# Optimization experiments

Measured on AMD Instinct MI355X. Metric: run time of the kernel, lower is better.

Reference implementation:

```python
import math
import jax, jax.numpy as jnp
import numpy as np

V, D, DEPTH, S, B = 32000, 1024, 4, 512, 2
N, K = 16, 4            # ssm state_dim, d_conv
R = math.ceil(D / 16)   # dt_rank ('auto') = 64
MLP = 4 * D


def _ln(x, s, b):
    m = jnp.mean(x, -1, keepdims=True)
    v = jnp.mean((x - m) ** 2, -1, keepdims=True)
    return (x - m) * jax.lax.rsqrt(v + 1e-5) * s + b


def _dwconv(x, w):
    # x: [B,S,D], w: [D,1,K]; causal depthwise conv (torch pads K-1 both sides then slices [:S])
    xt = jnp.transpose(x, (0, 2, 1))  # [B,D,S]
    y = jax.lax.conv_general_dilated(
        xt, w, window_strides=(1,), padding=[(K - 1, 0)],
        feature_group_count=D, dimension_numbers=('NCH', 'OIH', 'NCH'))
    return jnp.transpose(y, (0, 2, 1))


def _ssm(x, zw, pw, cw, dw, db, al, dpar, ow):
    z = x @ zw.T                     # [B,S,D]
    p = x @ pw.T                     # [B,S,R+2N]
    dt_un, Bp, Cp = p[..., :R], p[..., R:R + N], p[..., R + N:]
    dt = jax.nn.softplus(dt_un @ dw.T + db)          # [B,S,D]
    u = jax.nn.silu(_dwconv(x, cw))                  # [B,S,D]
    A = -jnp.exp(al)                                 # [D,N]
    At = jnp.exp(dt[..., None] * A)                  # [B,S,D,N]
    Bt = jnp.where(jnp.abs(A) < 1e-8, dt[..., None], (At - 1.0) / (A + 1e-10))
    inp = jnp.einsum('bsdn,bsn,bsd->bsdn', Bt, Bp, u)

    def step(h, xs):
        At_t, inp_t, C_t = xs
        h = At_t * h + inp_t
        return h, jnp.einsum('bn,bdn->bd', C_t, h)

    h0 = jnp.zeros((x.shape[0], D, N), x.dtype)
    _, ys = jax.lax.scan(step, h0, (jnp.moveaxis(At, 1, 0), jnp.moveaxis(inp, 1, 0), jnp.moveaxis(Cp, 1, 0)))
    y = jnp.moveaxis(ys, 0, 1)                       # [B,S,D]
    y = (y + u * dpar) * jax.nn.silu(z)
    return y @ ow.T


def _forward(input_ids, timesteps, tok_emb, time_w1, time_b1, time_w2, time_b2,
             norm1_s, norm1_b, xW, zW, pW, convW, dtW, dtb, A_log, Dp, outW,
             norm2_s, norm2_b, mlpW1, mlpb1, mlpW2, mlpb2, normo_s, normo_b, headW, headb):
    half = D // 2
    inv = jnp.exp(-(math.log(10000.0) / half) * jnp.arange(half, dtype=jnp.float32))
    args = timesteps.astype(jnp.float32)[:, None] * inv
    temb = jnp.concatenate([jnp.sin(args), jnp.cos(args)], axis=-1)        # [B,D]
    temb = jax.nn.silu(temb @ time_w1.T + time_b1) @ time_w2.T + time_b2
    x = tok_emb[input_ids] + temb[:, None, :]                              # [B,S,D]

    def block(x, prm):
        n1s, n1b, zw, pw, cw, dw, db, al, dpar, ow, n2s, n2b, w1, b1, w2, b2 = prm
        x = x + _ssm(_ln(x, n1s, n1b), zw, pw, cw, dw, db, al, dpar, ow)
        xn = _ln(x, n2s, n2b)
        x = x + (jax.nn.gelu(xn @ w1.T + b1, approximate=False) @ w2.T + b2)
        return x, None

    stacked = (norm1_s, norm1_b, zW, pW, convW, dtW, dtb, A_log, Dp, outW,
               norm2_s, norm2_b, mlpW1, mlpb1, mlpW2, mlpb2)
    x, _ = jax.lax.scan(block, x, stacked)
    x = _ln(x, normo_s, normo_b)
    return x @ headW.T + headb  # [B,S,V]


def setup_inputs():
    key = jax.random.key(0)
    ks = jax.random.split(key, 24)
    rn = lambda k, sh, sc=0.02: jax.random.normal(k, sh, jnp.float32) * sc
    dt_std = R ** (-0.5) * 0.1
    inp = {
        'input_ids': jax.random.randint(ks[0], (B, S), 0, V + 1),
        'timesteps': jax.random.randint(ks[1], (B,), 0, 100),
        'tok_emb': rn(ks[2], (V + 1, D)),
        'time_w1': rn(ks[3], (4 * D, D)), 'time_b1': jnp.zeros((4 * D,), jnp.float32),
        'time_w2': rn(ks[4], (D, 4 * D)), 'time_b2': jnp.zeros((D,), jnp.float32),
        'norm1_s': jnp.ones((DEPTH, D), jnp.float32), 'norm1_b': jnp.zeros((DEPTH, D), jnp.float32),
        'xW': rn(ks[5], (DEPTH, D, D)),   # in_proj_x (dead in forward, grad=0)
        'zW': rn(ks[6], (DEPTH, D, D)),
        'pW': rn(ks[7], (DEPTH, R + 2 * N, D)),
        'convW': rn(ks[8], (DEPTH, D, 1, K), 0.1),
        'dtW': jax.random.uniform(ks[9], (DEPTH, D, R), jnp.float32, -dt_std, dt_std),
        'dtb': jnp.full((DEPTH, D), math.log(math.expm1(0.001)), jnp.float32),
        'A_log': jnp.tile(jnp.log(jnp.arange(1, N + 1, dtype=jnp.float32))[None, None, :], (DEPTH, D, 1)),
        'Dp': jnp.ones((DEPTH, D), jnp.float32),
        'outW': rn(ks[10], (DEPTH, D, D)),
        'norm2_s': jnp.ones((DEPTH, D), jnp.float32), 'norm2_b': jnp.zeros((DEPTH, D), jnp.float32),
        'mlpW1': rn(ks[11], (DEPTH, MLP, D)), 'mlpb1': jnp.zeros((DEPTH, MLP), jnp.float32),
        'mlpW2': rn(ks[12], (DEPTH, D, MLP)), 'mlpb2': jnp.zeros((DEPTH, D), jnp.float32),
        'normo_s': jnp.ones((D,), jnp.float32), 'normo_b': jnp.zeros((D,), jnp.float32),
        'headW': rn(ks[13], (V, D)), 'headb': jnp.zeros((V,), jnp.float32),
    }
    return inp


def reference(input_ids, timesteps, tok_emb, time_w1, time_b1, time_w2, time_b2,
              norm1_s, norm1_b, xW, zW, pW, convW, dtW, dtb, A_log, Dp, outW,
              norm2_s, norm2_b, mlpW1, mlpb1, mlpW2, mlpb2, normo_s, normo_b, headW, headb):
    return _forward(input_ids, timesteps, tok_emb, time_w1, time_b1, time_w2, time_b2,
                    norm1_s, norm1_b, xW, zW, pW, convW, dtW, dtb, A_log, Dp, outW,
                    norm2_s, norm2_b, mlpW1, mlpb1, mlpW2, mlpb2, normo_s, normo_b, headW, headb)
```

## Files before the change

### kernel.cpp

```cpp
#include <hip/hip_runtime.h>
#include <math.h>


#define DEV __device__ __forceinline__
typedef unsigned int u32;
typedef unsigned short ushort;
typedef __bf16 bf16x8 __attribute__((ext_vector_type(8)));
typedef float f32x4 __attribute__((ext_vector_type(4)));
typedef ushort us8 __attribute__((ext_vector_type(8)));

DEV float silu_f(float x){ return x / (1.f + expf(-x)); }
DEV float gelu_f(float x){ return 0.5f * x * (1.f + erff(x * 0.70710678118654752f)); }
DEV float softplus_f(float x){ return (x > 20.f) ? x : log1pf(expf(x)); }
DEV ushort f2b(float f){
  u32 u = __builtin_bit_cast(u32, f);
  return (ushort)((u + 0x7fffu + ((u >> 16) & 1u)) >> 16);
}
DEV float b2f(ushort u){ return __builtin_bit_cast(float, (u32)u << 16); }

DEV void gl_lds16(const ushort* g, ushort* l){
  __builtin_amdgcn_global_load_lds(
      (const __attribute__((address_space(1))) u32*)g,
      (__attribute__((address_space(3))) u32*)l, 16, 0, 0);
}

DEV us8 cvt2(float4 a, float4 b){
  us8 v;
  v[0]=f2b(a.x); v[1]=f2b(a.y); v[2]=f2b(a.z); v[3]=f2b(a.w);
  v[4]=f2b(b.x); v[5]=f2b(b.y); v[6]=f2b(b.z); v[7]=f2b(b.w);
  return v;
}

DEV void cvt_layer_unit(u32 j, const float* zWl, const float* pWl, const float* oWl,
                        const float* m1Wl, const float* m2Wl, ushort* wl)
{
  const float* src; u32 sj, dj;
  if (j < 294912u){
    dj = j;
    u32 row = j >> 8;
    if (row < 1024u){ src = zWl; sj = j; }
    else {
      u32 pr = row - 1024u;
      if (pr >= 96u){ ushort4 z4 = {0,0,0,0}; ((ushort4*)wl)[dj] = z4; return; }
      src = pWl; sj = pr*256u + (j & 255u);
    }
  } else if (j < 557056u){ u32 k = j - 294912u;  dj = j; src = oWl;  sj = k; }
  else if (j < 1605632u){ u32 k = j - 557056u;  dj = j; src = m1Wl; sj = k; }
  else                  { u32 k = j - 1605632u; dj = j; src = m2Wl; sj = k; }
  float4 v = ((const float4*)src)[sj];
  ushort4 o4; o4.x=f2b(v.x); o4.y=f2b(v.y); o4.z=f2b(v.z); o4.w=f2b(v.w);
  ((ushort4*)wl)[dj] = o4;
}

__global__ __launch_bounds__(256) void k_cvtmega(
    const float* __restrict__ zW, const float* __restrict__ pW,
    const float* __restrict__ oW, const float* __restrict__ m1W,
    const float* __restrict__ m2W, ushort* __restrict__ wall)
{
  u32 i = blockIdx.x*256u + threadIdx.x;
  if (i >= 10616832u) return;
  u32 l = i / 2654208u;
  u32 j = i - l*2654208u;
  cvt_layer_unit(j, zW + (size_t)l*1048576u, pW + (size_t)l*98304u,
                 oW + (size_t)l*1048576u, m1W + (size_t)l*4194304u,
                 m2W + (size_t)l*4194304u, wall + (size_t)l*10616832u);
}

__global__ __launch_bounds__(256) void k_cvtall(
    const float* __restrict__ zWl, const float* __restrict__ pWl,
    const float* __restrict__ oWl, const float* __restrict__ m1Wl,
    const float* __restrict__ m2Wl, ushort* __restrict__ wl)
{
  u32 j = blockIdx.x*256u + threadIdx.x;
  if (j >= 2654208u) return;
  cvt_layer_unit(j, zWl, pWl, oWl, m1Wl, m2Wl, wl);
}

__global__ __launch_bounds__(256) void k_cvt(const float* __restrict__ in, ushort* __restrict__ out, int n4){
  int i = blockIdx.x*256 + threadIdx.x;
  if (i >= n4) return;
  float4 v = ((const float4*)in)[i];
  ushort4 o; o.x=f2b(v.x); o.y=f2b(v.y); o.z=f2b(v.z); o.w=f2b(v.w);
  ((ushort4*)out)[i] = o;
}

__global__ __launch_bounds__(256) void k_temb1m(const int* __restrict__ ts, const float* __restrict__ w1,
                                                const float* __restrict__ b1, float* __restrict__ t1){
  __shared__ float sXT[1024];
  int bid = blockIdx.x;
  int tid = threadIdx.x;
  int b = (bid*4) >> 12;
  float tv = (float)ts[b];
  #pragma unroll
  for (int k=0;k<4;k++){
    int j = tid + k*256;
    int i = j & 511;
    float arg = tv * expf(-(9.210340371976184f/512.f) * (float)i);
    sXT[j] = (j < 512) ? sinf(arg) : cosf(arg);
  }
  __syncthreads();
  int o = bid*4 + (tid >> 6);
  int lane = tid & 63;
  int j = o & 4095;
  const float4* xr = (const float4*)sXT;
  const float4* wr = (const float4*)(w1 + (size_t)j*1024);
  float acc = 0.f;
  #pragma unroll
  for (int i=0;i<4;i++){
    float4 x4 = xr[i*64 + lane], w4 = wr[i*64 + lane];
    acc += x4.x*w4.x + x4.y*w4.y + x4.z*w4.z + x4.w*w4.w;
  }
  #pragma unroll
  for (int off=32; off; off>>=1) acc += __shfl_down(acc, off);
  if (lane==0) t1[o] = silu_f(acc + b1[j]);
}

__global__ __launch_bounds__(256) void k_temb2(const float* __restrict__ t1, const float* __restrict__ w2,
                                               const float* __restrict__ b2, float* __restrict__ t2){
  int o = blockIdx.x*4 + (threadIdx.x >> 6);
  int lane = threadIdx.x & 63;
  int b = o >> 10, j = o & 1023;
  const float4* xr = (const float4*)(t1 + b*4096);
  const float4* wr = (const float4*)(w2 + (size_t)j*4096);
  float acc = 0.f;
  #pragma unroll
  for (int i=0;i<16;i++){
    float4 x4 = xr[i*64 + lane], w4 = wr[i*64 + lane];
    acc += x4.x*w4.x + x4.y*w4.y + x4.z*w4.z + x4.w*w4.w;
  }
  #pragma unroll
  for (int off=32; off; off>>=1) acc += __shfl_down(acc, off);
  if (lane==0) t2[o] = acc + b2[j];
}

DEV void ln_body(float4 v, const float* sc, const float* bi, int row, int t,
                 float* o, ushort* obf)
{
  float sum = v.x+v.y+v.z+v.w;
  float sq  = v.x*v.x+v.y*v.y+v.z*v.z+v.w*v.w;
  for (int o_=32;o_;o_>>=1){ sum += __shfl_down(sum,o_); sq += __shfl_down(sq,o_); }
  __shared__ float ps[8];
  int lane = t & 63, wid = t >> 6;
  if (lane==0){ ps[wid]=sum; ps[4+wid]=sq; }
  __syncthreads();
  float tot = ps[0]+ps[1]+ps[2]+ps[3];
  float tsq = ps[4]+ps[5]+ps[6]+ps[7];
  float m = tot * (1.f/1024.f);
  float var = tsq*(1.f/1024.f) - m*m;
  float r = rsqrtf(var + 1e-5f);
  float4 s4 = ((const float4*)sc)[t];
  float4 b4 = ((const float4*)bi)[t];
  float4 o4;
  o4.x = (v.x-m)*r*s4.x + b4.x;
  o4.y = (v.y-m)*r*s4.y + b4.y;
  o4.z = (v.z-m)*r*s4.z + b4.z;
  o4.w = (v.w-m)*r*s4.w + b4.w;
  ((float4*)(o + (size_t)row*1024))[t] = o4;
  ushort4 ob; ob.x=f2b(o4.x); ob.y=f2b(o4.y); ob.z=f2b(o4.z); ob.w=f2b(o4.w);
  ((ushort4*)(obf + (size_t)row*1024))[t] = ob;
}

__global__ __launch_bounds__(256) void k_ln(const float* __restrict__ x, const float* __restrict__ sc,
                                            const float* __restrict__ bi, float* __restrict__ o,
                                            ushort* __restrict__ obf){
  int row = blockIdx.x, t = threadIdx.x;
  float4 v = ((const float4*)(x + (size_t)row*1024))[t];
  ln_body(v, sc, bi, row, t, o, obf);
}

__global__ __launch_bounds__(256) void k_embln(const int* __restrict__ ids, const float* __restrict__ tok,
                                               const float* __restrict__ t2, const float* __restrict__ sc,
                                               const float* __restrict__ bi, float* __restrict__ xout,
                                               float* __restrict__ o, ushort* __restrict__ obf){
  int row = blockIdx.x, t = threadIdx.x;
  int id = ids[row];
  float4 v = ((const float4*)(tok + (size_t)id*1024))[t];
  float4 e = ((const float4*)(t2 + ((row >> 9) << 10)))[t];
  v.x += e.x; v.y += e.y; v.z += e.z; v.w += e.w;
  ((float4*)(xout + (size_t)row*1024))[t] = v;
  ln_body(v, sc, bi, row, t, o, obf);
}

__global__ __launch_bounds__(512) void k_scanf(
    const ushort* __restrict__ pb64, const float* __restrict__ dtW, const float* __restrict__ dtb,
    const float* __restrict__ xn, const float* __restrict__ p, const float* __restrict__ alog,
    const float* __restrict__ z, const float* __restrict__ Dp,
    const float* __restrict__ cw, ushort* __restrict__ y2b)
{
  const int bid = blockIdx.x;
  const int logical = (bid & 7)*256 + (bid >> 3);
  const int d = logical & 1023;
  const int b = logical >> 10;
  const int tid = threadIdx.x;
  const int c = tid >> 4, n = tid & 15;
  const float al = alog[d*16 + n];
  const float A = -expf(al);
  const float invA = 1.f/(A + 1e-10f);
  const bool tiny = fabsf(A) < 1e-8f;
  const float dscale = Dp[d];
  const float cw0 = cw[d*4], cw1 = cw[d*4+1], cw2 = cw[d*4+2], cw3 = cw[d*4+3];
  const size_t base = (size_t)b*512*1024 + d;
  const float* pp = p + (size_t)b*512*96;
  const int s0 = c*16;

  __shared__ float sXN[520];
  __shared__ float sDT[512], sZ[512];
  __shared__ float sA[512], sB[512], sH[512];
  __shared__ float sDTW[64];

  if (tid < 64) sDTW[tid] = dtW[d*64 + tid];
  {
    int s = tid - 3;
    sXN[tid] = (s >= 0) ? xn[base + (size_t)s*1024] : 0.f;
    if (tid < 3) sXN[512 + tid] = xn[base + (size_t)(509 + tid)*1024];
    sZ[tid] = z[base + (size_t)tid*1024];
  }
  __syncthreads();

  {
    const us8* pr = (const us8*)(pb64 + (size_t)(b*512 + tid)*64);
    float acc = 0.f;
    #pragma unroll
    for (int q=0;q<8;q++){
      us8 v = pr[q];
      #pragma unroll
      for (int e=0;e<8;e++)
        acc = fmaf(b2f(v[e]), sDTW[q*8+e], acc);
    }
    sDT[tid] = softplus_f(acc + dtb[d]);
  }
  __syncthreads();

  float At[16], inp[16];
  float h = 0.f, pa = 1.f;
  #pragma unroll
  for (int s8=0; s8<16; s8++){
    int s = s0 + s8;
    float uv = silu_f(sXN[s]*cw0 + sXN[s+1]*cw1 + sXN[s+2]*cw2 + sXN[s+3]*cw3);
    float dtv = sDT[s];
    float Bpv = pp[s*96 + 64 + n];
    float a  = expf(dtv*A);
    float bt = tiny ? dtv : (a-1.f)*invA;
    At[s8] = a;
    float ip = bt*Bpv*uv;
    inp[s8] = ip;
    h = a*h + ip;
    pa *= a;
  }
  sA[tid]=pa; sB[tid]=h;
  __syncthreads();
  if (tid < 16){
    float H = 0.f;
    #pragma unroll
    for (int c2=0;c2<32;c2++){
      sH[c2*16+tid] = H;
      H = sA[c2*16+tid]*H + sB[c2*16+tid];
    }
  }
  __syncthreads();

  h = sH[tid];
  #pragma unroll
  for (int s8=0; s8<16; s8++){
    int s = s0 + s8;
    h = At[s8]*h + inp[s8];
    float Cpv = pp[s*96 + 80 + n];
    float cc = Cpv*h;
    cc += __shfl_xor(cc,1);
    cc += __shfl_xor(cc,2);
    cc += __shfl_xor(cc,4);
    cc += __shfl_xor(cc,8);
    if (n==0){
      float uv = silu_f(sXN[s]*cw0 + sXN[s+1]*cw1 + sXN[s+2]*cw2 + sXN[s+3]*cw3);
      float zv = sZ[s];
      y2b[base + (size_t)s*1024] = f2b((cc + uv*dscale) * (zv/(1.f+expf(-zv))));
    }
  }
}

template<int TM, int TN, int EPI, bool OBF>
__global__ __launch_bounds__(256) void k_bgemm(
    const ushort* __restrict__ A,
    const ushort* __restrict__ W,
    const float* __restrict__ bias,
    const float* __restrict__ resid,
    void* __restrict__ Cout,
    int ldc, int nmax, int K,
    float* __restrict__ pout, ushort* __restrict__ pbout)
{
  constexpr int WN = 2;
  constexpr int WM = 2;
  constexpr int MR = TM/(WM*16);
  constexpr int NR = TN/(WN*16);

  __shared__ ushort As[TM*64] __attribute__((aligned(16)));
  __shared__ ushort Bs[TN*64] __attribute__((aligned(16)));
  const int t = threadIdx.x;
  const int w = t >> 6, lane = t & 63;
  const int wn = w % WN, wm = w / WN;
  const int m0 = blockIdx.y * TM;
  const int n0 = blockIdx.x * TN;

  f32x4 acc[MR][NR];
  #pragma unroll
  for (int i=0;i<MR;i++)
    #pragma unroll
    for (int j=0;j<NR;j++) acc[i][j] = (f32x4){0.f,0.f,0.f,0.f};

  const int srow = (lane >> 3);
  const int scol = (((lane & 7) ^ srow)) * 8;

  for (int k0 = 0; k0 < K; k0 += 64){
    __syncthreads();
    #pragma unroll
    for (int i=0;i<TM/32;i++){
      int chunk = i*4 + w;
      int row = chunk*8 + srow;
      gl_lds16(A + (size_t)(m0 + row)*K + k0 + scol, &As[chunk*512]);
    }
    #pragma unroll
    for (int i=0;i<TN/32;i++){
      int chunk = i*4 + w;
      int row = chunk*8 + srow;
      gl_lds16(W + (size_t)(n0 + row)*K + k0 + scol, &Bs[chunk*512]);
    }
    __syncthreads();
    const int fr = lane & 15;
    const int hi = lane >> 4;
    #pragma unroll
    for (int kk=0; kk<2; ++kk){
      bf16x8 a[MR], b[NR];
      const int cofs = (((kk<<2) | hi) ^ (fr & 7)) * 8;
      #pragma unroll
      for (int am=0; am<MR; am++)
        a[am] = *(const bf16x8*)&As[(wm*(MR*16) + am*16 + fr)*64 + cofs];
      #pragma unroll
      for (int bn=0; bn<NR; bn++)
        b[bn] = *(const bf16x8*)&Bs[(wn*(NR*16) + bn*16 + fr)*64 + cofs];
      #pragma unroll
      for (int am=0; am<MR; am++)
        #pragma unroll
        for (int bn=0; bn<NR; bn++)
          acc[am][bn] = __builtin_amdgcn_mfma_f32_16x16x32_bf16(a[am], b[bn], acc[am][bn], 0, 0, 0);
    }
  }

  #pragma unroll
  for (int am=0; am<MR; am++){
    #pragma unroll
    for (int bn=0; bn<NR; bn++){
      int r0 = m0 + wm*(MR*16) + am*16 + ((lane>>4)<<2);
      int cc = n0 + wn*(NR*16) + bn*16 + (lane&15);
      if (cc >= nmax) continue;
      float bv = 0.f;
      if constexpr (EPI==1 || EPI==2 || EPI==5) bv = bias[cc];
      #pragma unroll
      for (int r=0; r<4; r++){
        float v = acc[am][bn][r];
        if constexpr (EPI==1 || EPI==2 || EPI==5) v += bv;
        if constexpr (EPI==2) v = gelu_f(v);
        if constexpr (EPI==4 || EPI==5) v += resid[(size_t)(r0+r)*ldc + cc];
        if constexpr (EPI==6){
          if (cc < 1024) ((float*)Cout)[(size_t)(r0+r)*ldc + cc] = v;
          else {
            int pc = cc - 1024;
            if (pc < 96) pout[(size_t)(r0+r)*96 + pc] = v;
            if (pc < 64) pbout[(size_t)(r0+r)*64 + pc] = f2b(v);
          }
        } else if constexpr (OBF){
          ((ushort*)Cout)[(size_t)(r0+r)*ldc + cc] = f2b(v);
        } else {
          ((float*)Cout)[(size_t)(r0+r)*ldc + cc] = v;
        }
      }
    }
  }
}

__global__ __launch_bounds__(512) void k_bgemmHF(
    const ushort* __restrict__ A,
    const float*  __restrict__ W,
    const float* __restrict__ bias,
    float* __restrict__ Cout,
    int ldc, int K)
{
  __shared__ ushort As[256*64] __attribute__((aligned(16)));
  __shared__ ushort Bs[128*64] __attribute__((aligned(16)));
  const int t = threadIdx.x;
  const int w = t >> 6, lane = t & 63;
  const int wn = w & 1, wm = w >> 1;
  const int bid = blockIdx.x;
  const int logical = (bid & 7)*125 + (bid >> 3);
  const int m0 = (logical & 3) * 256;
  const int n0 = (logical >> 2) * 128;

  f32x4 acc[4][4];
  #pragma unroll
  for (int i=0;i<4;i++)
    #pragma unroll
    for (int j=0;j<4;j++) acc[i][j] = (f32x4){0.f,0.f,0.f,0.f};

  const int srow = (lane >> 3);
  const int scolA = (((lane & 7) ^ srow)) * 8;

  const int brow = t >> 2;
  const int bq   = t & 3;
  const float* wp = W + (size_t)(n0 + brow)*K + bq*16;
  const int slot0 = ((bq*2)   ^ (brow & 7)) * 8;
  const int slot1 = ((bq*2+1) ^ (brow & 7)) * 8;

  float4 fb[4];
  #pragma unroll
  for (int j=0;j<4;j++) fb[j] = *(const float4*)(wp + j*4);

  for (int k0 = 0; k0 < K; k0 += 64){
    __syncthreads();
    #pragma unroll
    for (int i=0;i<4;i++){
      int chunk = i*8 + w;
      int row = chunk*8 + srow;
      gl_lds16(A + (size_t)(m0 + row)*K + k0 + scolA, &As[chunk*512]);
    }
    *(us8*)&Bs[brow*64 + slot0] = cvt2(fb[0], fb[1]);
    *(us8*)&Bs[brow*64 + slot1] = cvt2(fb[2], fb[3]);
    if (k0 + 64 < K){
      #pragma unroll
      for (int j=0;j<4;j++) fb[j] = *(const float4*)(wp + k0 + 64 + j*4);
      asm volatile("s_waitcnt vmcnt(4) lgkmcnt(0)" ::: "memory");
    } else {
      asm volatile("s_waitcnt vmcnt(0) lgkmcnt(0)" ::: "memory");
    }
    __builtin_amdgcn_sched_barrier(0);
    __builtin_amdgcn_s_barrier();
    __builtin_amdgcn_sched_barrier(0);
    const int fr = lane & 15;
    const int hi = lane >> 4;
    #pragma unroll
    for (int kk=0; kk<2; ++kk){
      bf16x8 a[4], b[4];
      const int cofs = (((kk<<2) | hi) ^ (fr & 7)) * 8;
      #pragma unroll
      for (int am=0; am<4; am++)
        a[am] = *(const bf16x8*)&As[(wm*64 + am*16 + fr)*64 + cofs];
      #pragma unroll
      for (int bn=0; bn<4; bn++)
        b[bn] = *(const bf16x8*)&Bs[(wn*64 + bn*16 + fr)*64 + cofs];
      #pragma unroll
      for (int am=0; am<4; am++)
        #pragma unroll
        for (int bn=0; bn<4; bn++)
          acc[am][bn] = __builtin_amdgcn_mfma_f32_16x16x32_bf16(a[am], b[bn], acc[am][bn], 0, 0, 0);
    }
  }

  #pragma unroll
  for (int am=0; am<4; am++){
    #pragma unroll
    for (int bn=0; bn<4; bn++){
      int r0 = m0 + wm*64 + am*16 + ((lane>>4)<<2);
      int cc = n0 + wn*64 + bn*16 + (lane&15);
      float bv = bias[cc];
      #pragma unroll
      for (int r=0; r<4; r++)
        Cout[(size_t)(r0+r)*ldc + cc] = acc[am][bn][r] + bv;
    }
  }
}

extern "C" void kernel_launch(void* const* d_in, const int* in_sizes, int n_in,
                              void* d_out, int out_size, void* d_ws, size_t ws_size,
                              hipStream_t stream)
{
  const int*   ids    = (const int*)d_in[0];
  const int*   tsteps = (const int*)d_in[1];
  const float* tok    = (const float*)d_in[2];
  const float* tw1    = (const float*)d_in[3];
  const float* tb1    = (const float*)d_in[4];
  const float* tw2    = (const float*)d_in[5];
  const float* tb2    = (const float*)d_in[6];
  const float* n1s    = (const float*)d_in[7];
  const float* n1b    = (const float*)d_in[8];
  const float* zW     = (const float*)d_in[10];
  const float* pW     = (const float*)d_in[11];
  const float* cW     = (const float*)d_in[12];
  const float* dtW    = (const float*)d_in[13];
  const float* dtb    = (const float*)d_in[14];
  const float* alog   = (const float*)d_in[15];
  const float* Dp     = (const float*)d_in[16];
  const float* oW     = (const float*)d_in[17];
  const float* n2s    = (const float*)d_in[18];
  const float* n2b    = (const float*)d_in[19];
  const float* m1W    = (const float*)d_in[20];
  const float* m1b    = (const float*)d_in[21];
  const float* m2W    = (const float*)d_in[22];
  const float* m2b    = (const float*)d_in[23];
  const float* nos    = (const float*)d_in[24];
  const float* nob    = (const float*)d_in[25];
  const float* hW     = (const float*)d_in[26];
  const float* hb     = (const float*)d_in[27];

  float* ws = (float*)d_ws;
  float*  x    = ws;
  float*  xn   = ws + 1048576;
  float*  z    = ws + 2097152;
  float*  p    = ws + 3145728;
  ushort* pb64 = (ushort*)(ws + 3244032);
  float*  t1   = ws + 3276800;
  float*  t2   = ws + 3284992;
  ushort* xnb  = (ushort*)(ws + 3670016);
  ushort* y2b  = (ushort*)(ws + 4194304);
  ushort* h1b  = (ushort*)(ws + 5242880);

  const size_t WBASE = 7340032;
  const size_t WL_US = 10616832;
  const bool big = ws_size >= 179830784ull;
  ushort* wall = (ushort*)(ws + WBASE);
  ushort* whb  = (ushort*)(ws + WBASE + (big ? 4*(WL_US/2) : 0));

  dim3 blk(256);
  if (big)
    k_cvtmega<<<dim3(41472), blk, 0, stream>>>(zW, pW, oW, m1W, m2W, wall);
  k_temb1m<<<dim3(2048), blk, 0, stream>>>(tsteps, tw1, tb1, t1);
  k_temb2<<<dim3(512),  blk, 0, stream>>>(t1, tw2, tb2, t2);

  for (int l=0; l<4; l++){
    ushort* wl = wall + (big ? (size_t)l*WL_US : 0);
    ushort* wzp = wl;
    ushort* wo  = wl + 1179648;
    ushort* wm1 = wl + 2228224;
    ushort* wm2 = wl + 6422528;
    if (!big)
      k_cvtall<<<dim3(10368), blk, 0, stream>>>(
          zW + (size_t)l*1048576, pW + (size_t)l*98304, oW + (size_t)l*1048576,
          m1W + (size_t)l*4194304, m2W + (size_t)l*4194304, wl);
    if (l == 0)
      k_embln<<<dim3(1024), blk, 0, stream>>>(ids, tok, t2, n1s, n1b, x, xn, xnb);
    else
      k_ln<<<dim3(1024), blk, 0, stream>>>(x, n1s + l*1024, n1b + l*1024, xn, xnb);
    k_bgemm<64,64,6,false><<<dim3(18,16), blk, 0, stream>>>(xnb, wzp, nullptr, nullptr, z,
                                                            1024, 1152, 1024, p, pb64);
    k_scanf<<<dim3(2048), dim3(512), 0, stream>>>(pb64, dtW + (size_t)l*65536, dtb + l*1024,
                                                  xn, p, alog + l*16384, z, Dp + l*1024,
                                                  cW + l*4096, y2b);
    k_bgemm<64,64,4,false><<<dim3(16,16), blk, 0, stream>>>(y2b, wo, nullptr, x, x,
                                                            1024, 1024, 1024, nullptr, nullptr);
    k_ln<<<dim3(1024), blk, 0, stream>>>(x, n2s + l*1024, n2b + l*1024, xn, xnb);
    k_bgemm<64,64,2,true><<<dim3(64,16), blk, 0, stream>>>(xnb, wm1, m1b + l*4096, nullptr, h1b,
                                                           4096, 4096, 1024, nullptr, nullptr);
    k_bgemm<64,64,5,false><<<dim3(16,16), blk, 0, stream>>>(h1b, wm2, m2b + l*1024, x, x,
                                                            1024, 1024, 4096, nullptr, nullptr);
  }
  k_ln<<<dim3(1024), blk, 0, stream>>>(x, nos, nob, xn, xnb);

  if (big){
    k_bgemmHF<<<dim3(1000), dim3(512), 0, stream>>>(xnb, hW, hb, (float*)d_out, 32000, 1024);
  } else {
    for (int h=0; h<2; h++){
      k_cvt<<<dim3(16000), blk, 0, stream>>>(hW + (size_t)h*16384000, whb, 4096000);
      k_bgemm<128,128,1,false><<<dim3(125,8), blk, 0, stream>>>(xnb, whb, hb + h*16000, nullptr,
                                                                (float*)d_out + h*16000,
                                                                32000, 16000, 1024, nullptr, nullptr);
    }
  }
}
```

Measured before the change: 890.9 us.

## Double-buffer LDS tiles in bf16 GEMM to overlap global loads with MFMA

The GEMM kernel now keeps two LDS buffers per operand and issues the async global-to-LDS loads for the next K-step before computing on the current one. Explicit vmcnt waits and barriers replace the two __syncthreads per iteration. This is meant to hide global memory latency behind MFMA work, at the cost of twice the shared memory per block, which may reduce occupancy.

```diff
diff --git a/kernel.cpp b/kernel.cpp
--- a/kernel.cpp
+++ b/kernel.cpp
@@ -292,9 +292,12 @@
   constexpr int WM = 2;
   constexpr int MR = TM/(WM*16);
   constexpr int NR = TN/(WN*16);
-
-  __shared__ ushort As[TM*64] __attribute__((aligned(16)));
-  __shared__ ushort Bs[TN*64] __attribute__((aligned(16)));
+  constexpr int LA = TM/32;
+  constexpr int LB = TN/32;
+  constexpr int LT = LA + LB;
+
+  __shared__ ushort As[2][TM*64] __attribute__((aligned(16)));
+  __shared__ ushort Bs[2][TN*64] __attribute__((aligned(16)));
   const int t = threadIdx.x;
   const int w = t >> 6, lane = t & 63;
   const int wn = w % WN, wm = w / WN;
@@ -310,39 +313,54 @@
   const int srow = (lane >> 3);
   const int scol = (((lane & 7) ^ srow)) * 8;
 
-  for (int k0 = 0; k0 < K; k0 += 64){
-    __syncthreads();
-    #pragma unroll
-    for (int i=0;i<TM/32;i++){
+  auto issue = [&](int k0, int buf){
+    #pragma unroll
+    for (int i=0;i<LA;i++){
       int chunk = i*4 + w;
       int row = chunk*8 + srow;
-      gl_lds16(A + (size_t)(m0 + row)*K + k0 + scol, &As[chunk*512]);
-    }
-    #pragma unroll
-    for (int i=0;i<TN/32;i++){
+      gl_lds16(A + (size_t)(m0 + row)*K + k0 + scol, &As[buf][chunk*512]);
+    }
+    #pragma unroll
+    for (int i=0;i<LB;i++){
       int chunk = i*4 + w;
       int row = chunk*8 + srow;
-      gl_lds16(W + (size_t)(n0 + row)*K + k0 + scol, &Bs[chunk*512]);
-    }
-    __syncthreads();
-    const int fr = lane & 15;
-    const int hi = lane >> 4;
+      gl_lds16(W + (size_t)(n0 + row)*K + k0 + scol, &Bs[buf][chunk*512]);
+    }
+  };
+
+  issue(0, 0);
+  const int NS = K >> 6;
+  const int fr = lane & 15;
+  const int hi = lane >> 4;
+  for (int s = 0; s < NS; ++s){
+    const int cur = s & 1;
+    if (s + 1 < NS){
+      issue((s+1)*64, cur^1);
+      asm volatile("s_waitcnt vmcnt(%0)" :: "i"(LT) : "memory");
+    } else {
+      asm volatile("s_waitcnt vmcnt(0)" ::: "memory");
+    }
+    __builtin_amdgcn_sched_barrier(0);
+    __builtin_amdgcn_s_barrier();
+    __builtin_amdgcn_sched_barrier(0);
     #pragma unroll
     for (int kk=0; kk<2; ++kk){
       bf16x8 a[MR], b[NR];
       const int cofs = (((kk<<2) | hi) ^ (fr & 7)) * 8;
       #pragma unroll
       for (int am=0; am<MR; am++)
-        a[am] = *(const bf16x8*)&As[(wm*(MR*16) + am*16 + fr)*64 + cofs];
+        a[am] = *(const bf16x8*)&As[cur][(wm*(MR*16) + am*16 + fr)*64 + cofs];
       #pragma unroll
       for (int bn=0; bn<NR; bn++)
-        b[bn] = *(const bf16x8*)&Bs[(wn*(NR*16) + bn*16 + fr)*64 + cofs];
+        b[bn] = *(const bf16x8*)&Bs[cur][(wn*(NR*16) + bn*16 + fr)*64 + cofs];
       #pragma unroll
       for (int am=0; am<MR; am++)
         #pragma unroll
         for (int bn=0; bn<NR; bn++)
           acc[am][bn] = __builtin_amdgcn_mfma_f32_16x16x32_bf16(a[am], b[bn], acc[am][bn], 0, 0, 0);
     }
+    __builtin_amdgcn_sched_barrier(0);
+    __builtin_amdgcn_s_barrier();
   }
 
   #pragma unroll
```

New measurement: 879.3 us. No clear change (-1.3%).
